# Performance work log

Hardware: AMD Instinct MI355X
Metric: run time of the kernel (lower is better)

Reference implementation:

```python
import jax, jax.numpy as jnp
import numpy as np

HIDDEN = 64
N_HEADS = 4
TOP_K = 10
ALPHA = 0.3


def setup_inputs() -> dict:
    key = jax.random.key(0)
    ks = jax.random.split(key, 12)
    B, N, T, Dd, Ds, H = 4, 2048, 32, 16, 8, HIDDEN
    s = lambda i, shape, scale: (jax.random.normal(ks[i], shape, dtype=jnp.float32) * scale)
    return {
        "x_dyn": jax.random.normal(ks[0], (B, N, T, Dd), dtype=jnp.float32),
        "x_stat": jax.random.normal(ks[1], (B, N, Ds), dtype=jnp.float32),
        "A_prior": jax.random.uniform(ks[2], (B, N, N), dtype=jnp.float32),
        "W_dyn": s(3, (Dd, H), 1.0 / np.sqrt(Dd)),
        "b_dyn": jnp.zeros((H,), jnp.float32),
        "W_stat": s(4, (Ds, H), 1.0 / np.sqrt(Ds)),
        "b_stat": jnp.zeros((H,), jnp.float32),
        "W_fuse": s(5, (2 * H, H), 1.0 / np.sqrt(2 * H)),
        "b_fuse": jnp.zeros((H,), jnp.float32),
        "Wq": s(6, (H, H), 1.0 / np.sqrt(H)),
        "Wk": s(7, (H, H), 1.0 / np.sqrt(H)),
    }


def reference(x_dyn, x_stat, A_prior, W_dyn, b_dyn, W_stat, b_stat, W_fuse, b_fuse, Wq, Wk):
    B, N = x_dyn.shape[0], x_dyn.shape[1]
    H, nh = HIDDEN, N_HEADS
    dh = H // nh

    # TemporalEncoder: linear + mean over time + ReLU -> (B, N, H)
    h = jax.nn.relu(jnp.mean(x_dyn @ W_dyn + b_dyn, axis=2))
    # FeatureEncoder: linear + ReLU -> (B, N, H)
    h_s = jax.nn.relu(x_stat @ W_stat + b_stat)
    # Fusion
    h = jnp.concatenate([h, h_s], axis=-1) @ W_fuse + b_fuse

    # GraphAttention: multi-head softmax(QK^T / sqrt(dh)) averaged over heads
    q = (h @ Wq).reshape(B, N, nh, dh)
    k = (h @ Wk).reshape(B, N, nh, dh)
    scores = jnp.einsum("bnhd,bmhd->bhnm", q, k) / jnp.sqrt(jnp.float32(dh))
    A_learn = jnp.mean(jax.nn.softmax(scores, axis=-1), axis=1)  # (B, N, N)

    # Top-k mask along last dim (scatter 1s at topk indices)
    _, topk_inds = jax.lax.top_k(A_learn, TOP_K)  # (B, N, k)
    b_idx = jnp.arange(B)[:, None, None]
    n_idx = jnp.arange(N)[None, :, None]
    mask = jnp.zeros_like(A_learn).at[b_idx, n_idx, topk_inds].set(1.0)
    A_sparse = A_learn * mask
    A_learn = (A_sparse + jnp.swapaxes(A_sparse, 1, 2)) * 0.5

    # Blend with prior
    A_final = ALPHA * A_prior + (1.0 - ALPHA) * A_learn

    # Laplacian L = D - A
    degree = jnp.sum(A_final, axis=-1)  # (B, N)
    eye = jnp.eye(N, dtype=A_final.dtype)
    L = degree[..., None] * eye - A_final
    return (L, A_final)
```

## Files before the change

kernel.cpp:

```cpp
#include <hip/hip_runtime.h>

#define NBATCH 4
#define NN 2048
#define NR 8192
#define TOPK 10

typedef __attribute__((ext_vector_type(4))) float f32x4;
typedef __attribute__((ext_vector_type(8))) short bf16x8;

__device__ inline unsigned short f2bf(float x) {
    unsigned u = __float_as_uint(x);
    unsigned r = (u + 0x7FFF + ((u >> 16) & 1)) >> 16;
    return (unsigned short)r;
}

__global__ __launch_bounds__(256) void k1_encode(
    const float* __restrict__ xd, const float* __restrict__ xs,
    const float* __restrict__ Wd, const float* __restrict__ bd,
    const float* __restrict__ Ws, const float* __restrict__ bs,
    const float* __restrict__ Wf, const float* __restrict__ bf,
    const float* __restrict__ Wq, const float* __restrict__ Wk,
    unsigned short* __restrict__ qh, unsigned short* __restrict__ kh)
{
    int wave = threadIdx.x >> 6;
    int lane = threadIdx.x & 63;
    int r = blockIdx.x * 4 + wave;

    __shared__ float xm[4][16];
    __shared__ float xst[4][8];
    __shared__ float hc[4][128];
    __shared__ float hh[4][64];

    const float* xdr = xd + (size_t)r * 512;
    float acc = 0.f;
    #pragma unroll
    for (int j = 0; j < 8; ++j) acc += xdr[lane + 64*j];
    acc += __shfl_xor(acc, 16);
    acc += __shfl_xor(acc, 32);
    if (lane < 16) xm[wave][lane] = acc * (1.0f/32.0f);
    if (lane < 8)  xst[wave][lane] = xs[(size_t)r*8 + lane];
    __syncthreads();

    float a1 = bd[lane];
    #pragma unroll
    for (int d = 0; d < 16; ++d) a1 += xm[wave][d] * Wd[d*64 + lane];
    a1 = fmaxf(a1, 0.f);
    float a2 = bs[lane];
    #pragma unroll
    for (int d = 0; d < 8; ++d) a2 += xst[wave][d] * Ws[d*64 + lane];
    a2 = fmaxf(a2, 0.f);
    hc[wave][lane] = a1;
    hc[wave][64 + lane] = a2;
    __syncthreads();

    float hv0 = bf[lane], hv1 = 0.f, hv2 = 0.f, hv3 = 0.f;
    #pragma unroll
    for (int j = 0; j < 128; j += 4) {
        hv0 += hc[wave][j]   * Wf[(j)*64   + lane];
        hv1 += hc[wave][j+1] * Wf[(j+1)*64 + lane];
        hv2 += hc[wave][j+2] * Wf[(j+2)*64 + lane];
        hv3 += hc[wave][j+3] * Wf[(j+3)*64 + lane];
    }
    hh[wave][lane] = (hv0 + hv1) + (hv2 + hv3);
    __syncthreads();

    float qv0 = 0.f, qv1 = 0.f, kv0 = 0.f, kv1 = 0.f;
    #pragma unroll
    for (int j = 0; j < 64; j += 2) {
        float h0 = hh[wave][j], h1 = hh[wave][j+1];
        qv0 += h0 * Wq[(j)*64   + lane];
        qv1 += h1 * Wq[(j+1)*64 + lane];
        kv0 += h0 * Wk[(j)*64   + lane];
        kv1 += h1 * Wk[(j+1)*64 + lane];
    }
    float qv = qv0 + qv1, kv = kv0 + kv1;
    int b = r >> 11, n = r & 2047;
    int head = lane >> 4, dim = lane & 15;
    size_t base = ((size_t)(b*4 + head) * NN + n) * 32;
    qh[base + dim] = f2bf(qv);
    qh[base + 16 + dim] = 0;
    kh[base + dim] = f2bf(kv);
    kh[base + 16 + dim] = 0;
}

__global__ __launch_bounds__(256) void k2a_stats(
    const unsigned short* __restrict__ qh, const unsigned short* __restrict__ kh,
    float* __restrict__ Rf)
{
    const float C1 = 0.36067376022224085f;
    int bh = blockIdx.x >> 7;
    int rg = blockIdx.x & 127;
    int w = threadIdx.x >> 6, l = threadIdx.x & 63;
    int quad = l >> 4, lo = l & 15;

    bf16x8 afrag = *(const bf16x8*)(qh + ((size_t)bh * NN + rg*16 + lo) * 32 + quad*8);
    const unsigned short* kbase = kh + (size_t)bh * NN * 32;

    __shared__ float redA[4][16];

    float Sloc[4] = {0.f,0.f,0.f,0.f};
    for (int t = 0; t < 32; ++t) {
        int m0 = w*512 + t*16;
        bf16x8 bfrag = *(const bf16x8*)(kbase + (size_t)(m0 + lo) * 32 + quad*8);
        f32x4 acc = {0.f,0.f,0.f,0.f};
        acc = __builtin_amdgcn_mfma_f32_16x16x32_bf16(afrag, bfrag, acc, 0, 0, 0);
        #pragma unroll
        for (int rr = 0; rr < 4; ++rr) Sloc[rr] += exp2f(acc[rr] * C1);
    }
    #pragma unroll
    for (int d = 1; d <= 8; d <<= 1) {
        #pragma unroll
        for (int rr = 0; rr < 4; ++rr) Sloc[rr] += __shfl_xor(Sloc[rr], d);
    }
    if (lo == 0) {
        #pragma unroll
        for (int rr = 0; rr < 4; ++rr) redA[w][quad*4 + rr] = Sloc[rr];
    }
    __syncthreads();
    if (threadIdx.x < 16) {
        float S = redA[0][threadIdx.x] + redA[1][threadIdx.x]
                + redA[2][threadIdx.x] + redA[3][threadIdx.x];
        Rf[(size_t)bh * NN + rg*16 + threadIdx.x] = 1.0f / S;
    }
}

__global__ __launch_bounds__(256) void k3_base(
    const float* __restrict__ prior, float* __restrict__ Lout,
    float* __restrict__ Aout)
{
    int r = blockIdx.x;
    const float4* pr = (const float4*)(prior + (size_t)r * NN);
    float4* Ar = (float4*)(Aout + (size_t)r * NN);
    float4* Lr = (float4*)(Lout + (size_t)r * NN);
    float sum = 0.f;
    for (int i = threadIdx.x; i < NN/4; i += 256) {
        float4 p = pr[i];
        float4 a; a.x = 0.3f*p.x; a.y = 0.3f*p.y; a.z = 0.3f*p.z; a.w = 0.3f*p.w;
        Ar[i] = a;
        float4 lv; lv.x = -a.x; lv.y = -a.y; lv.z = -a.z; lv.w = -a.w;
        Lr[i] = lv;
        sum += a.x + a.y + a.z + a.w;
    }
    #pragma unroll
    for (int o = 32; o > 0; o >>= 1) sum += __shfl_down(sum, o);
    __shared__ float wsum[4];
    if ((threadIdx.x & 63) == 0) wsum[threadIdx.x >> 6] = sum;
    __syncthreads();
    if (threadIdx.x == 0) {
        float tot = wsum[0] + wsum[1] + wsum[2] + wsum[3];
        atomicAdd(&Lout[(size_t)r * NN + (r & 2047)], tot);
    }
}

__global__ __launch_bounds__(1024) void k2b_topk(
    const unsigned short* __restrict__ qh, const unsigned short* __restrict__ kh,
    const float* __restrict__ Rf,
    float* __restrict__ Lout, float* __restrict__ Aout)
{
    const float C1 = 0.36067376022224085f;
    int b  = blockIdx.x >> 7;
    int rg = blockIdx.x & 127;
    int tid = threadIdx.x;
    int w = tid >> 6, l = tid & 63;
    int quad = l >> 4, lo = l & 15;

    __shared__ unsigned short vt[16][2048];

    bf16x8 afrag[4];
    float r4[4][4];
    #pragma unroll
    for (int h = 0; h < 4; ++h) {
        int bh = b*4 + h;
        afrag[h] = *(const bf16x8*)(qh + ((size_t)bh * NN + rg*16 + lo) * 32 + quad*8);
        #pragma unroll
        for (int rr = 0; rr < 4; ++rr)
            r4[h][rr] = Rf[(size_t)bh * NN + rg*16 + quad*4 + rr] * 0.25f;
    }

    int swz_w = quad << 4;
    for (int t = 0; t < 8; ++t) {
        int m0 = w*128 + t*16;
        float vacc[4] = {0.f,0.f,0.f,0.f};
        #pragma unroll
        for (int h = 0; h < 4; ++h) {
            bf16x8 bfrag = *(const bf16x8*)(kh + ((size_t)(b*4+h) * NN + m0 + lo) * 32 + quad*8);
            f32x4 acc = {0.f,0.f,0.f,0.f};
            acc = __builtin_amdgcn_mfma_f32_16x16x32_bf16(afrag[h], bfrag, acc, 0, 0, 0);
            #pragma unroll
            for (int rr = 0; rr < 4; ++rr) {
                float e = exp2f(acc[rr] * C1);
                vacc[rr] = fmaf(e, r4[h][rr], vacc[rr]);
            }
        }
        #pragma unroll
        for (int rr = 0; rr < 4; ++rr)
            vt[quad*4 + rr][(m0 + lo) ^ swz_w] = f2bf(vacc[rr]);
    }
    __syncthreads();

    {
        int row = w;
        int swz = (row >> 2) << 4;
        unsigned tk[TOPK];
        #pragma unroll
        for (int s = 0; s < TOPK; ++s) tk[s] = 0u;
        for (int j = 0; j < 16; ++j) {
            int m1 = 2*l + 128*j;
            unsigned pair = *(const unsigned*)&vt[row][m1 ^ swz];
            unsigned key0 = (pair << 16)          | (unsigned)(2047 - m1);
            unsigned key1 = (pair & 0xFFFF0000u)  | (unsigned)(2046 - m1);
            if (key0 > tk[TOPK-1]) {
                unsigned ck = key0;
                #pragma unroll
                for (int s = 0; s < TOPK; ++s) {
                    bool ins = ck > tk[s];
                    unsigned o = tk[s];
                    tk[s] = ins ? ck : o;
                    ck    = ins ? o  : ck;
                }
            }
            if (key1 > tk[TOPK-1]) {
                unsigned ck = key1;
                #pragma unroll
                for (int s = 0; s < TOPK; ++s) {
                    bool ins = ck > tk[s];
                    unsigned o = tk[s];
                    tk[s] = ins ? ck : o;
                    ck    = ins ? o  : ck;
                }
            }
        }
        unsigned mykey = 0u;
        #pragma unroll 1
        for (int s = 0; s < TOPK; ++s) {
            unsigned kmax = tk[0];
            #pragma unroll
            for (int d = 1; d < 64; d <<= 1) {
                unsigned o = __shfl_xor(kmax, d);
                kmax = (o > kmax) ? o : kmax;
            }
            if (tk[0] == kmax) {
                #pragma unroll
                for (int q = 0; q < TOPK-1; ++q) tk[q] = tk[q+1];
                tk[TOPK-1] = 0u;
            }
            if (l == s) mykey = kmax;
        }

        if (l < TOPK) {
            float wv = 0.35f * __uint_as_float(mykey & 0xFFFF0000u);
            int j = 2047 - (int)(mykey & 0x7FFu);
            int n = rg*16 + row;
            size_t rbase = (size_t)(b*NN + n) * NN;
            size_t jbase = (size_t)(b*NN + j) * NN;
            atomicAdd(&Aout[rbase + j],  wv);
            atomicAdd(&Aout[jbase + n],  wv);
            atomicAdd(&Lout[rbase + j], -wv);
            atomicAdd(&Lout[jbase + n], -wv);
            atomicAdd(&Lout[jbase + j],  wv);
            atomicAdd(&Lout[rbase + n],  wv);
        }
    }
}

extern "C" void kernel_launch(void* const* d_in, const int* in_sizes, int n_in,
                              void* d_out, int out_size, void* d_ws, size_t ws_size,
                              hipStream_t stream)
{
    const float* xd    = (const float*)d_in[0];
    const float* xs    = (const float*)d_in[1];
    const float* prior = (const float*)d_in[2];
    const float* Wd    = (const float*)d_in[3];
    const float* bd    = (const float*)d_in[4];
    const float* Ws    = (const float*)d_in[5];
    const float* bs    = (const float*)d_in[6];
    const float* Wf    = (const float*)d_in[7];
    const float* bf    = (const float*)d_in[8];
    const float* Wq    = (const float*)d_in[9];
    const float* Wk    = (const float*)d_in[10];

    float* Lout = (float*)d_out;
    float* Aout = Lout + (size_t)NR * NN;

    unsigned short* qh = (unsigned short*)d_ws;
    unsigned short* kh = qh + (size_t)16 * NN * 32;
    float* Rf  = (float*)(kh + (size_t)16 * NN * 32);

    k1_encode<<<NR/4, 256, 0, stream>>>(xd, xs, Wd, bd, Ws, bs, Wf, bf, Wq, Wk, qh, kh);
    k2a_stats<<<16*128, 256, 0, stream>>>(qh, kh, Rf);
    k3_base<<<NR, 256, 0, stream>>>(prior, Lout, Aout);
    k2b_topk<<<NBATCH*128, 1024, 0, stream>>>(qh, kh, Rf, Lout, Aout);
}
```

Measured before the change: 336.5 us.

## Use 32x32x16 MFMA without zero-padded head dim in attention kernels

The q/k workspace drops the zero padding from 32 to 16 elements per row, halving its size and the global traffic to fill and read it. The stats and top-k kernels switch from 16x16x32 MFMA, which wasted half its K dimension on zeros, to 32x32x16 MFMA, which uses the full 16-element head dim and covers 32 query rows per block. The top-k kernel now stages 32 rows in LDS with a padded row stride in place of the XOR swizzle, and each wave processes two rows. This halves the number of blocks, cuts the wasted MFMA work, and needs more LDS per block.

```diff
diff --git a/kernel.cpp b/kernel.cpp
--- a/kernel.cpp
+++ b/kernel.cpp
@@ -4,8 +4,10 @@
 #define NN 2048
 #define NR 8192
 #define TOPK 10
+#define COLSW 2054
 
 typedef __attribute__((ext_vector_type(4))) float f32x4;
+typedef __attribute__((ext_vector_type(16))) float f32x16;
 typedef __attribute__((ext_vector_type(8))) short bf16x8;
 
 __device__ inline unsigned short f2bf(float x) {
@@ -76,11 +78,9 @@
     float qv = qv0 + qv1, kv = kv0 + kv1;
     int b = r >> 11, n = r & 2047;
     int head = lane >> 4, dim = lane & 15;
-    size_t base = ((size_t)(b*4 + head) * NN + n) * 32;
+    size_t base = ((size_t)(b*4 + head) * NN + n) * 16;
     qh[base + dim] = f2bf(qv);
-    qh[base + 16 + dim] = 0;
     kh[base + dim] = f2bf(kv);
-    kh[base + 16 + dim] = 0;
 }
 
 __global__ __launch_bounds__(256) void k2a_stats(
@@ -88,39 +88,32 @@
     float* __restrict__ Rf)
 {
     const float C1 = 0.36067376022224085f;
-    int bh = blockIdx.x >> 7;
-    int rg = blockIdx.x & 127;
+    int bh = blockIdx.x >> 6;
+    int rg = blockIdx.x & 63;
     int w = threadIdx.x >> 6, l = threadIdx.x & 63;
-    int quad = l >> 4, lo = l & 15;
-
-    bf16x8 afrag = *(const bf16x8*)(qh + ((size_t)bh * NN + rg*16 + lo) * 32 + quad*8);
-    const unsigned short* kbase = kh + (size_t)bh * NN * 32;
-
-    __shared__ float redA[4][16];
-
-    float Sloc[4] = {0.f,0.f,0.f,0.f};
-    for (int t = 0; t < 32; ++t) {
-        int m0 = w*512 + t*16;
-        bf16x8 bfrag = *(const bf16x8*)(kbase + (size_t)(m0 + lo) * 32 + quad*8);
-        f32x4 acc = {0.f,0.f,0.f,0.f};
-        acc = __builtin_amdgcn_mfma_f32_16x16x32_bf16(afrag, bfrag, acc, 0, 0, 0);
-        #pragma unroll
-        for (int rr = 0; rr < 4; ++rr) Sloc[rr] += exp2f(acc[rr] * C1);
-    }
-    #pragma unroll
-    for (int d = 1; d <= 8; d <<= 1) {
-        #pragma unroll
-        for (int rr = 0; rr < 4; ++rr) Sloc[rr] += __shfl_xor(Sloc[rr], d);
-    }
-    if (lo == 0) {
-        #pragma unroll
-        for (int rr = 0; rr < 4; ++rr) redA[w][quad*4 + rr] = Sloc[rr];
-    }
-    __syncthreads();
-    if (threadIdx.x < 16) {
-        float S = redA[0][threadIdx.x] + redA[1][threadIdx.x]
-                + redA[2][threadIdx.x] + redA[3][threadIdx.x];
-        Rf[(size_t)bh * NN + rg*16 + threadIdx.x] = 1.0f / S;
+    int row = l & 31, khalf = l >> 5;
+
+    bf16x8 qfrag = *(const bf16x8*)(qh + ((size_t)bh * NN + rg*32 + row) * 16 + khalf*8);
+    const unsigned short* kbase = kh + (size_t)bh * NN * 16;
+
+    __shared__ float redS[4][32];
+
+    float Sloc = 0.f;
+    for (int t = 0; t < 16; ++t) {
+        int m0 = w*512 + t*32;
+        bf16x8 kfrag = *(const bf16x8*)(kbase + (size_t)(m0 + row) * 16 + khalf*8);
+        f32x16 acc = {0.f,0.f,0.f,0.f,0.f,0.f,0.f,0.f,0.f,0.f,0.f,0.f,0.f,0.f,0.f,0.f};
+        acc = __builtin_amdgcn_mfma_f32_32x32x16_bf16(kfrag, qfrag, acc, 0, 0, 0);
+        #pragma unroll
+        for (int rr = 0; rr < 16; ++rr) Sloc += exp2f(acc[rr] * C1);
+    }
+    Sloc += __shfl_xor(Sloc, 32);
+    if (l < 32) redS[w][l] = Sloc;
+    __syncthreads();
+    if (threadIdx.x < 32) {
+        float S = redS[0][threadIdx.x] + redS[1][threadIdx.x]
+                + redS[2][threadIdx.x] + redS[3][threadIdx.x];
+        Rf[(size_t)bh * NN + rg*32 + threadIdx.x] = 1.0f / S;
     }
 }
 
@@ -152,61 +145,62 @@
     }
 }
 
-__global__ __launch_bounds__(1024) void k2b_topk(
+__global__ __launch_bounds__(1024, 4) void k2b_topk(
     const unsigned short* __restrict__ qh, const unsigned short* __restrict__ kh,
     const float* __restrict__ Rf,
     float* __restrict__ Lout, float* __restrict__ Aout)
 {
     const float C1 = 0.36067376022224085f;
-    int b  = blockIdx.x >> 7;
-    int rg = blockIdx.x & 127;
+    int b  = blockIdx.x >> 6;
+    int rg = blockIdx.x & 63;
     int tid = threadIdx.x;
     int w = tid >> 6, l = tid & 63;
-    int quad = l >> 4, lo = l & 15;
-
-    __shared__ unsigned short vt[16][2048];
-
-    bf16x8 afrag[4];
-    float r4[4][4];
+    int row = l & 31, khalf = l >> 5;
+
+    __shared__ unsigned short vt[32][COLSW];
+
+    bf16x8 qfrag[4];
+    float r4[4];
     #pragma unroll
     for (int h = 0; h < 4; ++h) {
         int bh = b*4 + h;
-        afrag[h] = *(const bf16x8*)(qh + ((size_t)bh * NN + rg*16 + lo) * 32 + quad*8);
-        #pragma unroll
-        for (int rr = 0; rr < 4; ++rr)
-            r4[h][rr] = Rf[(size_t)bh * NN + rg*16 + quad*4 + rr] * 0.25f;
-    }
-
-    int swz_w = quad << 4;
-    for (int t = 0; t < 8; ++t) {
-        int m0 = w*128 + t*16;
-        float vacc[4] = {0.f,0.f,0.f,0.f};
+        qfrag[h] = *(const bf16x8*)(qh + ((size_t)bh * NN + rg*32 + row) * 16 + khalf*8);
+        r4[h] = Rf[(size_t)bh * NN + rg*32 + row] * 0.25f;
+    }
+
+    for (int t = 0; t < 4; ++t) {
+        int m0 = w*128 + t*32;
+        float vacc[16];
+        #pragma unroll
+        for (int rr = 0; rr < 16; ++rr) vacc[rr] = 0.f;
         #pragma unroll
         for (int h = 0; h < 4; ++h) {
-            bf16x8 bfrag = *(const bf16x8*)(kh + ((size_t)(b*4+h) * NN + m0 + lo) * 32 + quad*8);
-            f32x4 acc = {0.f,0.f,0.f,0.f};
-            acc = __builtin_amdgcn_mfma_f32_16x16x32_bf16(afrag[h], bfrag, acc, 0, 0, 0);
+            bf16x8 kfrag = *(const bf16x8*)(kh + ((size_t)(b*4+h) * NN + m0 + row) * 16 + khalf*8);
+            f32x16 acc = {0.f,0.f,0.f,0.f,0.f,0.f,0.f,0.f,0.f,0.f,0.f,0.f,0.f,0.f,0.f,0.f};
+            acc = __builtin_amdgcn_mfma_f32_32x32x16_bf16(kfrag, qfrag[h], acc, 0, 0, 0);
             #pragma unroll
-            for (int rr = 0; rr < 4; ++rr) {
-                float e = exp2f(acc[rr] * C1);
-                vacc[rr] = fmaf(e, r4[h][rr], vacc[rr]);
-            }
-        }
-        #pragma unroll
-        for (int rr = 0; rr < 4; ++rr)
-            vt[quad*4 + rr][(m0 + lo) ^ swz_w] = f2bf(vacc[rr]);
-    }
-    __syncthreads();
-
-    {
-        int row = w;
-        int swz = (row >> 2) << 4;
+            for (int rr = 0; rr < 16; ++rr)
+                vacc[rr] = fmaf(exp2f(acc[rr] * C1), r4[h], vacc[rr]);
+        }
+        #pragma unroll
+        for (int p = 0; p < 8; ++p) {
+            int reg0 = p*2;
+            int c = m0 + ((reg0 & 3) + 8*(reg0 >> 2) + 4*khalf);
+            unsigned pk = (unsigned)f2bf(vacc[reg0]) | ((unsigned)f2bf(vacc[reg0+1]) << 16);
+            *(unsigned*)&vt[row][c] = pk;
+        }
+    }
+    __syncthreads();
+
+    #pragma unroll 1
+    for (int rr2 = 0; rr2 < 2; ++rr2) {
+        int prow = w*2 + rr2;
         unsigned tk[TOPK];
         #pragma unroll
         for (int s = 0; s < TOPK; ++s) tk[s] = 0u;
         for (int j = 0; j < 16; ++j) {
             int m1 = 2*l + 128*j;
-            unsigned pair = *(const unsigned*)&vt[row][m1 ^ swz];
+            unsigned pair = *(const unsigned*)&vt[prow][m1];
             unsigned key0 = (pair << 16)          | (unsigned)(2047 - m1);
             unsigned key1 = (pair & 0xFFFF0000u)  | (unsigned)(2046 - m1);
             if (key0 > tk[TOPK-1]) {
@@ -250,7 +244,7 @@
         if (l < TOPK) {
             float wv = 0.35f * __uint_as_float(mykey & 0xFFFF0000u);
             int j = 2047 - (int)(mykey & 0x7FFu);
-            int n = rg*16 + row;
+            int n = rg*32 + prow;
             size_t rbase = (size_t)(b*NN + n) * NN;
             size_t jbase = (size_t)(b*NN + j) * NN;
             atomicAdd(&Aout[rbase + j],  wv);
@@ -283,11 +277,11 @@
     float* Aout = Lout + (size_t)NR * NN;
 
     unsigned short* qh = (unsigned short*)d_ws;
-    unsigned short* kh = qh + (size_t)16 * NN * 32;
-    float* Rf  = (float*)(kh + (size_t)16 * NN * 32);
+    unsigned short* kh = qh + (size_t)16 * NN * 16;
+    float* Rf  = (float*)(kh + (size_t)16 * NN * 16);
 
     k1_encode<<<NR/4, 256, 0, stream>>>(xd, xs, Wd, bd, Ws, bs, Wf, bf, Wq, Wk, qh, kh);
-    k2a_stats<<<16*128, 256, 0, stream>>>(qh, kh, Rf);
+    k2a_stats<<<16*64, 256, 0, stream>>>(qh, kh, Rf);
     k3_base<<<NR, 256, 0, stream>>>(prior, Lout, Aout);
-    k2b_topk<<<NBATCH*128, 1024, 0, stream>>>(qh, kh, Rf, Lout, Aout);
-}
+    k2b_topk<<<NBATCH*64, 1024, 0, stream>>>(qh, kh, Rf, Lout, Aout);
+}
```

Result: faster. 328.5 us (-2.4%).
